# Optimization experiments

Hardware: AMD Instinct MI355X
Metric: run time of the kernel (lower is better)

## Reference

```python
import jax, jax.numpy as jnp
import numpy as np

B, C, H, W = 4, 64, 96, 96
KS, NH = 7, 4


def setup_inputs() -> dict:
    key = jax.random.key(0)
    ks = jax.random.split(key, 9)
    s = 0.1  # keep logits in a sane range for softmax
    return {
        "input_x": jax.random.normal(ks[0], (B, C, H, W), jnp.float32),
        "q_w": jax.random.normal(ks[1], (C, C), jnp.float32) * s,
        "q_b": jax.random.normal(ks[2], (C,), jnp.float32) * s,
        "k_w": jax.random.normal(ks[3], (C, C), jnp.float32) * s,
        "k_b": jax.random.normal(ks[4], (C,), jnp.float32) * s,
        "v_w": jax.random.normal(ks[5], (C, C), jnp.float32) * s,
        "v_b": jax.random.normal(ks[6], (C,), jnp.float32) * s,
        "rel_h": jax.random.normal(ks[7], (C // 2, KS, 1), jnp.float32) * s,
        "rel_w": jax.random.normal(ks[8], (C // 2, 1, KS), jnp.float32) * s,
    }


def _unfold(x, ks):
    # x: (B, C, Hp, Wp) -> (B, C, Ho, Wo, ks, ks), same as torch .unfold(2).unfold(3)
    Hp, Wp = x.shape[2], x.shape[3]
    Ho, Wo = Hp - ks + 1, Wp - ks + 1
    ih = jnp.arange(Ho)[:, None] + jnp.arange(ks)[None, :]  # (Ho, ks)
    iw = jnp.arange(Wo)[:, None] + jnp.arange(ks)[None, :]  # (Wo, ks)
    return x[:, :, ih[:, None, :, None], iw[None, :, None, :]]


def reference(input_x, q_w, q_b, k_w, k_b, v_w, v_b, rel_h, rel_w):
    b, c, h, w = input_x.shape
    ks, nh = KS, NH
    dkh = c // nh
    p0 = (ks - 1) // 2
    p1 = ks - 1 - p0
    padded = jnp.pad(input_x, ((0, 0), (0, 0), (p0, p1), (p0, p1)))

    conv1x1 = lambda x, wt, bi: jnp.einsum('bchw,oc->bohw', x, wt) + bi[None, :, None, None]
    k = conv1x1(padded, k_w, k_b)
    v = conv1x1(padded, v_w, v_b)
    q = conv1x1(input_x, q_w, q_b)

    # flat reshapes exactly as in torch (row-major), reproducing its layout semantics
    k = _unfold(k, ks).reshape(b, nh, h, w, dkh, ks * ks)
    v = _unfold(v, ks).reshape(b, nh, h, w, dkh, ks * ks)
    q = q.reshape(b, nh, h, w, dkh)  # torch: (b,nh,h,w,dkh,1) squeezed

    qk = jnp.einsum('bnxyd,bnxydk->bnxyk', q, k).reshape(b, nh, h, w, ks, ks)
    # torch einsum 'bhxydz,cij->bhxyij' == (sum_d q) outer (sum_c rel)
    qsum = q.sum(-1)  # (b, nh, h, w)
    rel = rel_h.sum(0) + rel_w.sum(0)  # broadcasts to (ks, ks)
    qk = qk + qsum[..., None, None] * rel

    weights = jax.nn.softmax(qk.reshape(b, nh, h, w, ks * ks), axis=-1)
    attn = jnp.einsum('bnxyk,bnxydk->bnxyd', weights, v)  # (b, nh, h, w, dkh)
    attn = attn.reshape(b, c, h, w)  # flat reshape, matching torch
    return jax.nn.relu(attn)
```

## Files before the change

### kernel.cpp

```cpp
#include <hip/hip_runtime.h>

#define B_ 4
#define C_ 64
#define H_ 96
#define W_ 96
#define KS_ 7
#define PH_ 102
#define PSTR 104
#define PHW (PH_ * PSTR)
#define NPIX (H_ * W_)
#define LDSTR 108

typedef __attribute__((ext_vector_type(8))) short short8;
typedef __attribute__((ext_vector_type(4))) float f32x4;

static __device__ inline ushort f2bf(float f) {
    union { float f; unsigned u; } v; v.f = f;
    unsigned r = (v.u + 0x7fff + ((v.u >> 16) & 1)) >> 16;
    return (ushort)r;
}


__global__ __launch_bounds__(256) void prep_kernel(
    const float* __restrict__ qw, const float* __restrict__ qb,
    const float* __restrict__ kw, const float* __restrict__ kb,
    const float* __restrict__ vw, const float* __restrict__ vb,
    ushort* __restrict__ wbf, float* __restrict__ bias_all,
    float* __restrict__ outk, float* __restrict__ outv)
{
    const int gid = blockIdx.x * 256 + threadIdx.x;
    if (blockIdx.x < 48) {
        const int idx = gid;
        const float* src = (idx < 4096) ? qw : (idx < 8192 ? kw : vw);
        wbf[idx] = f2bf(src[idx & 4095]);
        if (idx < 192) {
            const float* bsrc = (idx < 64) ? qb : (idx < 128 ? kb : vb);
            bias_all[idx] = bsrc[idx & 63];
        }
        return;
    }
    int item = gid - 48 * 256;
    if (item >= B_ * 2 * C_ * 1188) return;
    const int bp   = item % 1188;
    int rest       = item / 1188;
    const int ch   = rest % C_;
    rest /= C_;
    const int mode = rest & 1;
    const int b    = rest >> 1;
    int ph, pw;
    if (bp < 306)      { ph = bp / 102;              pw = bp % 102; }
    else if (bp < 612) { int j = bp - 306; ph = 99 + j / 102; pw = j % 102; }
    else               { int j = bp - 612; ph = 3 + j / 6; int c2 = j % 6;
                         pw = (c2 < 3) ? c2 : 96 + c2 - 3 + 3; }
    const float bias = (mode ? vb : kb)[ch];
    float* dst = mode ? outv : outk;
    dst[((size_t)b * C_ + ch) * PHW + ph * PSTR + pw] = bias;
}

__global__ __launch_bounds__(256) void mfma_conv_kernel(
    const float* __restrict__ in,
    const ushort* __restrict__ wbf,
    const float* __restrict__ bias_all,
    float* __restrict__ outq, float* __restrict__ outk, float* __restrict__ outv)
{
    const int b    = blockIdx.y;
    const int pix0 = blockIdx.x * 64;
    const int t    = threadIdx.x;
    const int lane = t & 63;
    const int wv   = t >> 6;

    __shared__ ushort xs[64 * 64];

    {
        const int pix = t & 63;
        const int cg  = t >> 6;
        const float* xp = in + (size_t)b * C_ * NPIX + pix0 + pix;
        #pragma unroll
        for (int g = 0; g < 4; ++g) {
            const int ch = (cg + 4 * g) * 4;
            float x0 = xp[(size_t)(ch    ) * NPIX];
            float x1 = xp[(size_t)(ch + 1) * NPIX];
            float x2 = xp[(size_t)(ch + 2) * NPIX];
            float x3 = xp[(size_t)(ch + 3) * NPIX];
            ushort4 u = make_ushort4(f2bf(x0), f2bf(x1), f2bf(x2), f2bf(x3));
            unsigned byte = (unsigned)(pix * 128 + ch * 2) ^ (unsigned)((pix & 7) << 4);
            *reinterpret_cast<ushort4*>(reinterpret_cast<char*>(xs) + byte) = u;
        }
    }
    __syncthreads();

    short8 afr[3][2];
    #pragma unroll
    for (int i = 0; i < 3; ++i) {
        const int row = (3 * wv + i) * 16 + (lane & 15);
        #pragma unroll
        for (int ka = 0; ka < 2; ++ka) {
            const int kk = ka * 32 + (lane >> 4) * 8;
            afr[i][ka] = *reinterpret_cast<const short8*>(wbf + row * 64 + kk);
        }
    }
    short8 bfr[4][2];
    #pragma unroll
    for (int nt = 0; nt < 4; ++nt) {
        const int pl = nt * 16 + (lane & 15);
        #pragma unroll
        for (int ka = 0; ka < 2; ++ka) {
            const int kk = ka * 32 + (lane >> 4) * 8;
            unsigned byte = (unsigned)(pl * 128 + kk * 2) ^ (unsigned)((pl & 7) << 4);
            bfr[nt][ka] = *reinterpret_cast<const short8*>(
                reinterpret_cast<const char*>(xs) + byte);
        }
    }
    f32x4 acc[3][4];
    #pragma unroll
    for (int i = 0; i < 3; ++i) {
        const int mt = 3 * wv + i;
        f32x4 bi;
        #pragma unroll
        for (int r = 0; r < 4; ++r) bi[r] = bias_all[mt * 16 + (lane >> 4) * 4 + r];
        #pragma unroll
        for (int nt = 0; nt < 4; ++nt) acc[i][nt] = bi;
    }
    #pragma unroll
    for (int i = 0; i < 3; ++i) {
        #pragma unroll
        for (int nt = 0; nt < 4; ++nt) {
            acc[i][nt] = __builtin_amdgcn_mfma_f32_16x16x32_bf16(
                afr[i][0], bfr[nt][0], acc[i][nt], 0, 0, 0);
            acc[i][nt] = __builtin_amdgcn_mfma_f32_16x16x32_bf16(
                afr[i][1], bfr[nt][1], acc[i][nt], 0, 0, 0);
        }
    }
    #pragma unroll
    for (int nt = 0; nt < 4; ++nt) {
        const int pix  = pix0 + nt * 16 + (lane & 15);
        const int h    = pix / 96;
        const int w    = pix - h * 96;
        const int ppix = (h + 3) * PSTR + (w + 3);
        #pragma unroll
        for (int i = 0; i < 3; ++i) {
            const int mt   = 3 * wv + i;
            const int mode = mt >> 2;
            const int ocb  = (mt & 3) * 16 + (lane >> 4) * 4;
            #pragma unroll
            for (int r = 0; r < 4; ++r) {
                const float val = acc[i][nt][r];
                if (mode == 0)
                    outq[((size_t)b * C_ + ocb + r) * NPIX + pix] = val;
                else if (mode == 1)
                    outk[((size_t)b * C_ + ocb + r) * PHW + ppix] = val;
                else
                    outv[((size_t)b * C_ + ocb + r) * PHW + ppix] = val;
            }
        }
    }
}

__global__ __launch_bounds__(384) void attn_kernel(
    const float* __restrict__ q, const float* __restrict__ k,
    const float* __restrict__ v, const float* __restrict__ relh,
    const float* __restrict__ relw, float* __restrict__ out)
{
    const int bx   = blockIdx.x;
    const int tile = bx % 3;
    const int c    = (bx / 3) % C_;
    const int b    = bx / (3 * C_);
    const int ho0  = tile * 32;
    const int t    = threadIdx.x;

    __shared__ float ks[38 * LDSTR];
    __shared__ float vs[38 * LDSTR];
    __shared__ float rel_s[49];

    if (t < 49) {
        const int i = t / KS_, j = t % KS_;
        float s = 0.f;
        #pragma unroll
        for (int cc = 0; cc < C_ / 2; ++cc)
            s += relh[cc * KS_ + i] + relw[cc * KS_ + j];
        rel_s[t] = s;
    }
    {
        const float* kp = k + ((size_t)(b * C_ + c) * PH_ + ho0) * PSTR;
        const float* vp = v + ((size_t)(b * C_ + c) * PH_ + ho0) * PSTR;
        for (int idx = t; idx < 38 * 26; idx += 384) {
            const int r = idx / 26, col = (idx % 26) * 4;
            *reinterpret_cast<float4*>(&ks[r * LDSTR + col]) =
                *reinterpret_cast<const float4*>(kp + r * PSTR + col);
            *reinterpret_cast<float4*>(&vs[r * LDSTR + col]) =
                *reinterpret_cast<const float4*>(vp + r * PSTR + col);
        }
    }
    __syncthreads();

    const int r0   = t / 12;
    const int rest = t % 12;
    const int w0   = (rest >> 1) * 16;
    const int half = rest & 1;
    const int ho   = ho0 + r0;

    const float* qp = q + (((size_t)b * C_ + c) * H_ + ho) * W_ + w0;
    float qs[16];
    #pragma unroll
    for (int tt = 0; tt < 16; tt += 4) {
        float4 f = *reinterpret_cast<const float4*>(qp + tt);
        qs[tt] = f.x; qs[tt + 1] = f.y; qs[tt + 2] = f.z; qs[tt + 3] = f.w;
    }
    float qsum = 0.f;
    #pragma unroll
    for (int tt = 0; tt < 16; ++tt) qsum += qs[tt];

    float logit[49];
    #pragma unroll
    for (int i = 0; i < KS_; ++i) {
        float kr[22];
        const float* kp = &ks[(r0 + i) * LDSTR + w0];
        #pragma unroll
        for (int tt = 0; tt < 20; tt += 4) {
            float4 f = *reinterpret_cast<const float4*>(kp + tt);
            kr[tt] = f.x; kr[tt + 1] = f.y; kr[tt + 2] = f.z; kr[tt + 3] = f.w;
        }
        float2 f2 = *reinterpret_cast<const float2*>(kp + 20);
        kr[20] = f2.x; kr[21] = f2.y;
        #pragma unroll
        for (int j = 0; j < KS_; ++j) {
            float s = 0.f;
            #pragma unroll
            for (int tt = 0; tt < 16; ++tt) s = fmaf(qs[tt], kr[tt + j], s);
            logit[i * KS_ + j] = s + qsum * rel_s[i * KS_ + j];
        }
    }

    float m = -1e30f;
    #pragma unroll
    for (int kk = 0; kk < 49; ++kk) m = fmaxf(m, logit[kk]);
    float ssum = 0.f;
    #pragma unroll
    for (int kk = 0; kk < 49; ++kk) {
        float e = __expf(logit[kk] - m);
        logit[kk] = e;
        ssum += e;
    }
    const float inv = 1.f / ssum;

    float o8[8];
    #pragma unroll
    for (int d = 0; d < 8; ++d) o8[d] = 0.f;

    #pragma unroll
    for (int i = 0; i < KS_; ++i) {
        float vr[14];
        const float* vp = &vs[(r0 + i) * LDSTR + w0 + half * 8];
        #pragma unroll
        for (int tt = 0; tt < 12; tt += 4) {
            float4 f = *reinterpret_cast<const float4*>(vp + tt);
            vr[tt] = f.x; vr[tt + 1] = f.y; vr[tt + 2] = f.z; vr[tt + 3] = f.w;
        }
        float2 f2 = *reinterpret_cast<const float2*>(vp + 12);
        vr[12] = f2.x; vr[13] = f2.y;
        #pragma unroll
        for (int j = 0; j < KS_; ++j) {
            float wgt = logit[i * KS_ + j];
            #pragma unroll
            for (int d = 0; d < 8; ++d) o8[d] = fmaf(wgt, vr[d + j], o8[d]);
        }
    }

    float* op = out + (((size_t)b * C_ + c) * H_ + ho) * W_ + w0 + half * 8;
    #pragma unroll
    for (int d = 0; d < 8; d += 4) {
        float4 f;
        f.x = fmaxf(o8[d]     * inv, 0.f);
        f.y = fmaxf(o8[d + 1] * inv, 0.f);
        f.z = fmaxf(o8[d + 2] * inv, 0.f);
        f.w = fmaxf(o8[d + 3] * inv, 0.f);
        *reinterpret_cast<float4*>(op + d) = f;
    }
}

extern "C" void kernel_launch(void* const* d_in, const int* in_sizes, int n_in,
                              void* d_out, int out_size, void* d_ws, size_t ws_size,
                              hipStream_t stream) {
    const float* in   = (const float*)d_in[0];
    const float* qw   = (const float*)d_in[1];
    const float* qb   = (const float*)d_in[2];
    const float* kw   = (const float*)d_in[3];
    const float* kb   = (const float*)d_in[4];
    const float* vw   = (const float*)d_in[5];
    const float* vb   = (const float*)d_in[6];
    const float* relh = (const float*)d_in[7];
    const float* relw = (const float*)d_in[8];
    float* out = (float*)d_out;

    float*  wk  = (float*)d_ws;
    float*  wvv = wk  + (size_t)B_ * C_ * PHW;
    float*  wq  = wvv + (size_t)B_ * C_ * PHW;
    ushort* wbf = (ushort*)(wq + (size_t)B_ * C_ * NPIX);
    float*  wbias = (float*)(wbf + 192 * 64);

    prep_kernel<<<48 + 2376, 256, 0, stream>>>(qw, qb, kw, kb, vw, vb,
                                               wbf, wbias, wk, wvv);

    dim3 cgrid(NPIX / 64, B_);
    mfma_conv_kernel<<<cgrid, 256, 0, stream>>>(in, wbf, wbias, wq, wk, wvv);

    dim3 agrid(B_ * C_ * 3);
    attn_kernel<<<agrid, 384, 0, stream>>>(wq, wk, wvv, relh, relw, out);
}
```

Measured before the change: 41.88 us.

## Drop prep kernel, fuse weight conversion into conv, synthesize K/V padding in attention

```diff
diff --git a/kernel.cpp b/kernel.cpp
--- a/kernel.cpp
+++ b/kernel.cpp
@@ -5,9 +5,6 @@
 #define H_ 96
 #define W_ 96
 #define KS_ 7
-#define PH_ 102
-#define PSTR 104
-#define PHW (PH_ * PSTR)
 #define NPIX (H_ * W_)
 #define LDSTR 108
 
@@ -21,63 +18,46 @@
 }
 
 
-__global__ __launch_bounds__(256) void prep_kernel(
+__global__ __launch_bounds__(256) void mfma_conv_kernel(
+    const float* __restrict__ in,
     const float* __restrict__ qw, const float* __restrict__ qb,
     const float* __restrict__ kw, const float* __restrict__ kb,
     const float* __restrict__ vw, const float* __restrict__ vb,
-    ushort* __restrict__ wbf, float* __restrict__ bias_all,
-    float* __restrict__ outk, float* __restrict__ outv)
-{
-    const int gid = blockIdx.x * 256 + threadIdx.x;
-    if (blockIdx.x < 48) {
-        const int idx = gid;
-        const float* src = (idx < 4096) ? qw : (idx < 8192 ? kw : vw);
-        wbf[idx] = f2bf(src[idx & 4095]);
-        if (idx < 192) {
-            const float* bsrc = (idx < 64) ? qb : (idx < 128 ? kb : vb);
-            bias_all[idx] = bsrc[idx & 63];
-        }
-        return;
-    }
-    int item = gid - 48 * 256;
-    if (item >= B_ * 2 * C_ * 1188) return;
-    const int bp   = item % 1188;
-    int rest       = item / 1188;
-    const int ch   = rest % C_;
-    rest /= C_;
-    const int mode = rest & 1;
-    const int b    = rest >> 1;
-    int ph, pw;
-    if (bp < 306)      { ph = bp / 102;              pw = bp % 102; }
-    else if (bp < 612) { int j = bp - 306; ph = 99 + j / 102; pw = j % 102; }
-    else               { int j = bp - 612; ph = 3 + j / 6; int c2 = j % 6;
-                         pw = (c2 < 3) ? c2 : 96 + c2 - 3 + 3; }
-    const float bias = (mode ? vb : kb)[ch];
-    float* dst = mode ? outv : outk;
-    dst[((size_t)b * C_ + ch) * PHW + ph * PSTR + pw] = bias;
-}
-
-__global__ __launch_bounds__(256) void mfma_conv_kernel(
-    const float* __restrict__ in,
-    const ushort* __restrict__ wbf,
-    const float* __restrict__ bias_all,
-    float* __restrict__ outq, float* __restrict__ outk, float* __restrict__ outv)
+    float* __restrict__ qkv)
 {
     const int b    = blockIdx.y;
-    const int pix0 = blockIdx.x * 64;
+    const int pix0 = blockIdx.x * 32;
     const int t    = threadIdx.x;
     const int lane = t & 63;
     const int wv   = t >> 6;
 
-    __shared__ ushort xs[64 * 64];
-
+    __shared__ ushort wlds[192 * 64];
+    __shared__ ushort xs[32 * 64];
+    __shared__ float  bias_s[192];
+
+    #pragma unroll
+    for (int g = 0; g < 12; ++g) {
+        const int qq  = t + 256 * g;
+        const int row = qq >> 4;
+        const int c4  = (qq & 15) * 4;
+        const float* src = (row < 64) ? qw + row * 64
+                         : (row < 128) ? kw + (row - 64) * 64
+                                       : vw + (row - 128) * 64;
+        float4 f = *reinterpret_cast<const float4*>(src + c4);
+        ushort4 u = make_ushort4(f2bf(f.x), f2bf(f.y), f2bf(f.z), f2bf(f.w));
+        unsigned byte = (unsigned)(row * 128 + c4 * 2) ^ (unsigned)((row & 7) << 4);
+        *reinterpret_cast<ushort4*>(reinterpret_cast<char*>(wlds) + byte) = u;
+    }
+    if (t < 192) {
+        const int tensor = t >> 6;
+        bias_s[t] = (tensor == 0 ? qb : tensor == 1 ? kb : vb)[t & 63];
+    }
     {
-        const int pix = t & 63;
-        const int cg  = t >> 6;
+        const int pix = t & 31, cg = t >> 5;
         const float* xp = in + (size_t)b * C_ * NPIX + pix0 + pix;
         #pragma unroll
-        for (int g = 0; g < 4; ++g) {
-            const int ch = (cg + 4 * g) * 4;
+        for (int g = 0; g < 2; ++g) {
+            const int ch = (cg + 8 * g) * 4;
             float x0 = xp[(size_t)(ch    ) * NPIX];
             float x1 = xp[(size_t)(ch + 1) * NPIX];
             float x2 = xp[(size_t)(ch + 2) * NPIX];
@@ -96,12 +76,14 @@
         #pragma unroll
         for (int ka = 0; ka < 2; ++ka) {
             const int kk = ka * 32 + (lane >> 4) * 8;
-            afr[i][ka] = *reinterpret_cast<const short8*>(wbf + row * 64 + kk);
-        }
-    }
-    short8 bfr[4][2];
-    #pragma unroll
-    for (int nt = 0; nt < 4; ++nt) {
+            unsigned byte = (unsigned)(row * 128 + kk * 2) ^ (unsigned)((row & 7) << 4);
+            afr[i][ka] = *reinterpret_cast<const short8*>(
+                reinterpret_cast<const char*>(wlds) + byte);
+        }
+    }
+    short8 bfr[2][2];
+    #pragma unroll
+    for (int nt = 0; nt < 2; ++nt) {
         const int pl = nt * 16 + (lane & 15);
         #pragma unroll
         for (int ka = 0; ka < 2; ++ka) {
@@ -111,20 +93,20 @@
                 reinterpret_cast<const char*>(xs) + byte);
         }
     }
-    f32x4 acc[3][4];
-    #pragma unroll
-    for (int i = 0; i < 3; ++i) {
-        const int mt = 3 * wv + i;
+    f32x4 acc[3][2];
+    #pragma unroll
+    for (int i = 0; i < 3; ++i) {
         f32x4 bi;
         #pragma unroll
-        for (int r = 0; r < 4; ++r) bi[r] = bias_all[mt * 16 + (lane >> 4) * 4 + r];
-        #pragma unroll
-        for (int nt = 0; nt < 4; ++nt) acc[i][nt] = bi;
-    }
-    #pragma unroll
-    for (int i = 0; i < 3; ++i) {
-        #pragma unroll
-        for (int nt = 0; nt < 4; ++nt) {
+        for (int r = 0; r < 4; ++r)
+            bi[r] = bias_s[(3 * wv + i) * 16 + (lane >> 4) * 4 + r];
+        #pragma unroll
+        for (int nt = 0; nt < 2; ++nt) acc[i][nt] = bi;
+    }
+    #pragma unroll
+    for (int i = 0; i < 3; ++i) {
+        #pragma unroll
+        for (int nt = 0; nt < 2; ++nt) {
             acc[i][nt] = __builtin_amdgcn_mfma_f32_16x16x32_bf16(
                 afr[i][0], bfr[nt][0], acc[i][nt], 0, 0, 0);
             acc[i][nt] = __builtin_amdgcn_mfma_f32_16x16x32_bf16(
@@ -132,34 +114,23 @@
         }
     }
     #pragma unroll
-    for (int nt = 0; nt < 4; ++nt) {
-        const int pix  = pix0 + nt * 16 + (lane & 15);
-        const int h    = pix / 96;
-        const int w    = pix - h * 96;
-        const int ppix = (h + 3) * PSTR + (w + 3);
-        #pragma unroll
-        for (int i = 0; i < 3; ++i) {
-            const int mt   = 3 * wv + i;
-            const int mode = mt >> 2;
-            const int ocb  = (mt & 3) * 16 + (lane >> 4) * 4;
+    for (int i = 0; i < 3; ++i) {
+        #pragma unroll
+        for (int r = 0; r < 4; ++r) {
+            const int row = (3 * wv + i) * 16 + (lane >> 4) * 4 + r;
+            float* op = qkv + ((size_t)b * 192 + row) * NPIX + pix0 + (lane & 15);
             #pragma unroll
-            for (int r = 0; r < 4; ++r) {
-                const float val = acc[i][nt][r];
-                if (mode == 0)
-                    outq[((size_t)b * C_ + ocb + r) * NPIX + pix] = val;
-                else if (mode == 1)
-                    outk[((size_t)b * C_ + ocb + r) * PHW + ppix] = val;
-                else
-                    outv[((size_t)b * C_ + ocb + r) * PHW + ppix] = val;
-            }
+            for (int nt = 0; nt < 2; ++nt)
+                op[nt * 16] = acc[i][nt][r];
         }
     }
 }
 
 __global__ __launch_bounds__(384) void attn_kernel(
-    const float* __restrict__ q, const float* __restrict__ k,
-    const float* __restrict__ v, const float* __restrict__ relh,
-    const float* __restrict__ relw, float* __restrict__ out)
+    const float* __restrict__ qkv,
+    const float* __restrict__ kb, const float* __restrict__ vb,
+    const float* __restrict__ relh, const float* __restrict__ relw,
+    float* __restrict__ out)
 {
     const int bx   = blockIdx.x;
     const int tile = bx % 3;
@@ -181,14 +152,17 @@
         rel_s[t] = s;
     }
     {
-        const float* kp = k + ((size_t)(b * C_ + c) * PH_ + ho0) * PSTR;
-        const float* vp = v + ((size_t)(b * C_ + c) * PH_ + ho0) * PSTR;
-        for (int idx = t; idx < 38 * 26; idx += 384) {
-            const int r = idx / 26, col = (idx % 26) * 4;
-            *reinterpret_cast<float4*>(&ks[r * LDSTR + col]) =
-                *reinterpret_cast<const float4*>(kp + r * PSTR + col);
-            *reinterpret_cast<float4*>(&vs[r * LDSTR + col]) =
-                *reinterpret_cast<const float4*>(vp + r * PSTR + col);
+        const float kbias = kb[c];
+        const float vbias = vb[c];
+        const float* kg = qkv + ((size_t)b * 192 +  64 + c) * NPIX;
+        const float* vg = qkv + ((size_t)b * 192 + 128 + c) * NPIX;
+        for (int idx = t; idx < 38 * 104; idx += 384) {
+            const int rl = idx / 104, cl = idx - rl * 104;
+            const int gr = ho0 + rl - 3, gc = cl - 3;
+            const bool inb = (gr >= 0 && gr < H_ && gc >= 0 && gc < W_);
+            const int gi = gr * W_ + gc;
+            ks[rl * LDSTR + cl] = inb ? kg[gi] : kbias;
+            vs[rl * LDSTR + cl] = inb ? vg[gi] : vbias;
         }
     }
     __syncthreads();
@@ -199,7 +173,7 @@
     const int half = rest & 1;
     const int ho   = ho0 + r0;
 
-    const float* qp = q + (((size_t)b * C_ + c) * H_ + ho) * W_ + w0;
+    const float* qp = qkv + ((size_t)b * 192 + c) * NPIX + ho * W_ + w0;
     float qs[16];
     #pragma unroll
     for (int tt = 0; tt < 16; tt += 4) {
@@ -224,24 +198,42 @@
         kr[20] = f2.x; kr[21] = f2.y;
         #pragma unroll
         for (int j = 0; j < KS_; ++j) {
-            float s = 0.f;
+            float s0 = 0.f, s1 = 0.f, s2 = 0.f, s3 = 0.f;
             #pragma unroll
-            for (int tt = 0; tt < 16; ++tt) s = fmaf(qs[tt], kr[tt + j], s);
-            logit[i * KS_ + j] = s + qsum * rel_s[i * KS_ + j];
-        }
-    }
-
-    float m = -1e30f;
-    #pragma unroll
-    for (int kk = 0; kk < 49; ++kk) m = fmaxf(m, logit[kk]);
-    float ssum = 0.f;
-    #pragma unroll
-    for (int kk = 0; kk < 49; ++kk) {
-        float e = __expf(logit[kk] - m);
-        logit[kk] = e;
-        ssum += e;
-    }
-    const float inv = 1.f / ssum;
+            for (int tt = 0; tt < 16; tt += 4) {
+                s0 = fmaf(qs[tt],     kr[tt + j],     s0);
+                s1 = fmaf(qs[tt + 1], kr[tt + 1 + j], s1);
+                s2 = fmaf(qs[tt + 2], kr[tt + 2 + j], s2);
+                s3 = fmaf(qs[tt + 3], kr[tt + 3 + j], s3);
+            }
+            logit[i * KS_ + j] = (s0 + s1) + (s2 + s3) + qsum * rel_s[i * KS_ + j];
+        }
+    }
+
+    float m0 = logit[0], m1 = logit[1], m2 = logit[2], m3 = logit[3];
+    #pragma unroll
+    for (int kk = 4; kk < 48; kk += 4) {
+        m0 = fmaxf(m0, logit[kk]);
+        m1 = fmaxf(m1, logit[kk + 1]);
+        m2 = fmaxf(m2, logit[kk + 2]);
+        m3 = fmaxf(m3, logit[kk + 3]);
+    }
+    float m = fmaxf(fmaxf(m0, m1), fmaxf(m2, m3));
+    m = fmaxf(m, logit[48]);
+
+    float e0 = 0.f, e1 = 0.f, e2 = 0.f, e3 = 0.f;
+    #pragma unroll
+    for (int kk = 0; kk < 48; kk += 4) {
+        float a0 = __expf(logit[kk]     - m);
+        float a1 = __expf(logit[kk + 1] - m);
+        float a2 = __expf(logit[kk + 2] - m);
+        float a3 = __expf(logit[kk + 3] - m);
+        logit[kk] = a0; logit[kk + 1] = a1; logit[kk + 2] = a2; logit[kk + 3] = a3;
+        e0 += a0; e1 += a1; e2 += a2; e3 += a3;
+    }
+    float a48 = __expf(logit[48] - m);
+    logit[48] = a48;
+    const float inv = 1.f / ((e0 + e1) + (e2 + e3) + a48);
 
     float o8[8];
     #pragma unroll
@@ -292,18 +284,11 @@
     const float* relw = (const float*)d_in[8];
     float* out = (float*)d_out;
 
-    float*  wk  = (float*)d_ws;
-    float*  wvv = wk  + (size_t)B_ * C_ * PHW;
-    float*  wq  = wvv + (size_t)B_ * C_ * PHW;
-    ushort* wbf = (ushort*)(wq + (size_t)B_ * C_ * NPIX);
-    float*  wbias = (float*)(wbf + 192 * 64);
-
-    prep_kernel<<<48 + 2376, 256, 0, stream>>>(qw, qb, kw, kb, vw, vb,
-                                               wbf, wbias, wk, wvv);
-
-    dim3 cgrid(NPIX / 64, B_);
-    mfma_conv_kernel<<<cgrid, 256, 0, stream>>>(in, wbf, wbias, wq, wk, wvv);
+    float* qkv = (float*)d_ws;
+
+    dim3 cgrid(NPIX / 32, B_);
+    mfma_conv_kernel<<<cgrid, 256, 0, stream>>>(in, qw, qb, kw, kb, vw, vb, qkv);
 
     dim3 agrid(B_ * C_ * 3);
-    attn_kernel<<<agrid, 384, 0, stream>>>(wq, wk, wvv, relh, relw, out);
-}
+    attn_kernel<<<agrid, 384, 0, stream>>>(qkv, kb, vb, relh, relw, out);
+}
```

Result: slower. 44.29 us (+5.8%).
